# Kernel tuning notes

Measured on AMD Instinct MI355X. Metric: run time of the kernel, lower is better.

## Reference

```python
import jax, jax.numpy as jnp
import numpy as np

ALPHA = 0.2  # LeakyReLU negative slope
NEG_INF = -9e15


def setup_inputs() -> dict:
    key = jax.random.key(0)
    k1, k2, k3, k4 = jax.random.split(key, 4)
    N, IN_F, OUT_F = 8192, 512, 256
    h = jax.random.normal(k1, (N, IN_F), dtype=jnp.float32)
    adj = jax.random.randint(k2, (N, N), 0, 2).astype(jnp.float32)
    # xavier_uniform for torch Linear weights
    limW = float(np.sqrt(6.0 / (IN_F + OUT_F)))
    W = jax.random.uniform(k3, (OUT_F, IN_F), dtype=jnp.float32, minval=-limW, maxval=limW)
    lima = float(np.sqrt(6.0 / (2 * OUT_F + 1)))
    a_vec = jax.random.uniform(k4, (2 * OUT_F,), dtype=jnp.float32, minval=-lima, maxval=lima)
    return {"h": h, "adj": adj, "W": W, "a_vec": a_vec}


def reference(h, adj, W, a_vec):
    # Wh = W(h), torch Linear: h @ W.T  -> [N, out]
    Wh = h @ W.T
    F_out = W.shape[0]
    # e_ij = leakyrelu(a . [Wh_i, Wh_j]) = leakyrelu(a1.Wh_i + a2.Wh_j)
    s_src = Wh @ a_vec[:F_out]   # [N] contribution of row i
    s_dst = Wh @ a_vec[F_out:]   # [N] contribution of col j
    e = jax.nn.leaky_relu(s_src[:, None] + s_dst[None, :], negative_slope=ALPHA)  # [N, N]
    scores = jnp.where(adj > 0, e, jnp.float32(NEG_INF))
    attention = jax.nn.softmax(scores, axis=1)
    # dropout is identity in eval mode
    h_prime = attention @ Wh  # [N, out]
    return h_prime, attention
```

## Files before the change

### kernel.cpp

```cpp
#include <hip/hip_runtime.h>
#include <stdint.h>

#define N_NODES 8192
#define IN_F    512
#define OUT_F   256
#define ALPHA   0.2f

typedef __attribute__((ext_vector_type(8))) short bf16x8;
typedef __attribute__((ext_vector_type(4))) float f32x4;

__device__ __forceinline__ uint32_t f32_to_bf16(float f) {
    union { float f; uint32_t u; } v; v.f = f;
    uint32_t u = v.u;
    return (u + 0x7fffu + ((u >> 16) & 1u)) >> 16;
}

__device__ __forceinline__ void async_copy16(const void* g, void* l) {
    __builtin_amdgcn_global_load_lds(
        (const __attribute__((address_space(1))) uint32_t*)g,
        (__attribute__((address_space(3))) uint32_t*)l, 16, 0, 0);
}

__global__ __launch_bounds__(256) void k0_wvec(
    const float* __restrict__ W, const float* __restrict__ a_vec,
    float* __restrict__ w12)
{
    const int t  = threadIdx.x;
    const int nb = blockIdx.x * 8;
    float a1lo = 0.f, a1hi = 0.f, a2lo = 0.f, a2hi = 0.f;
    #pragma unroll
    for (int q = 0; q < 8; q++) {
        int n = nb + q;
        float lo = W[(size_t)n * IN_F + t];
        float hi = W[(size_t)n * IN_F + t + 256];
        float a1 = a_vec[n], a2 = a_vec[OUT_F + n];
        a1lo = fmaf(lo, a1, a1lo); a1hi = fmaf(hi, a1, a1hi);
        a2lo = fmaf(lo, a2, a2lo); a2hi = fmaf(hi, a2, a2hi);
    }
    atomicAdd(&w12[t], a1lo);       atomicAdd(&w12[t + 256], a1hi);
    atomicAdd(&w12[512 + t], a2lo); atomicAdd(&w12[512 + t + 256], a2hi);
}

__global__ __launch_bounds__(256) void ks_svec(
    const float* __restrict__ h, const float* __restrict__ w12,
    float* __restrict__ s_src, float* __restrict__ s_dst)
{
    __shared__ float sw[1024];
    const int t = threadIdx.x;
    #pragma unroll
    for (int q = 0; q < 4; q++) sw[q * 256 + t] = w12[q * 256 + t];
    __syncthreads();
    const int w = t >> 6, ln = t & 63;
    const int i = blockIdx.x * 4 + w;
    const float* hr = h + (size_t)i * IN_F + ln * 8;
    float4 h0 = *(const float4*)hr;
    float4 h1 = *(const float4*)(hr + 4);
    const float* w1 = sw + ln * 8;
    const float* w2 = sw + 512 + ln * 8;
    float v1 = h0.x*w1[0] + h0.y*w1[1] + h0.z*w1[2] + h0.w*w1[3]
             + h1.x*w1[4] + h1.y*w1[5] + h1.z*w1[6] + h1.w*w1[7];
    float v2 = h0.x*w2[0] + h0.y*w2[1] + h0.z*w2[2] + h0.w*w2[3]
             + h1.x*w2[4] + h1.y*w2[5] + h1.z*w2[6] + h1.w*w2[7];
    #pragma unroll
    for (int off = 32; off >= 1; off >>= 1) {
        v1 += __shfl_xor(v1, off, 64);
        v2 += __shfl_xor(v2, off, 64);
    }
    if (ln == 0) { s_src[i] = v1; s_dst[i] = v2; }
}

__global__ __launch_bounds__(256) void k1_wh_pack(
    const float* __restrict__ h, const float* __restrict__ W,
    uint16_t* __restrict__ whf)
{
    const int n0 = blockIdx.x * 64, i0 = blockIdx.y * 64;
    const int t  = threadIdx.x;
    const int tn = t & 15, tm = t >> 4;

    __shared__ float As[32][68];
    __shared__ float Bs[32][68];

    float acc[4][4];
    #pragma unroll
    for (int i = 0; i < 4; i++)
        #pragma unroll
        for (int j = 0; j < 4; j++) acc[i][j] = 0.f;

    for (int k0 = 0; k0 < IN_F; k0 += 32) {
        __syncthreads();
        #pragma unroll
        for (int q = 0; q < 2; q++) {
            int u   = q * 256 + t;
            int row = u >> 3;
            int kf  = (u & 7) * 4;
            float4 va = *(const float4*)&h[(size_t)(i0 + row) * IN_F + k0 + kf];
            As[kf + 0][row] = va.x; As[kf + 1][row] = va.y;
            As[kf + 2][row] = va.z; As[kf + 3][row] = va.w;
            float4 vb = *(const float4*)&W[(size_t)(n0 + row) * IN_F + k0 + kf];
            Bs[kf + 0][row] = vb.x; Bs[kf + 1][row] = vb.y;
            Bs[kf + 2][row] = vb.z; Bs[kf + 3][row] = vb.w;
        }
        __syncthreads();
        #pragma unroll
        for (int kk = 0; kk < 32; kk++) {
            float a[4], b[4];
            *(float4*)a = *(const float4*)&As[kk][tm * 4];
            *(float4*)b = *(const float4*)&Bs[kk][tn * 4];
            #pragma unroll
            for (int i = 0; i < 4; i++)
                #pragma unroll
                for (int j = 0; j < 4; j++) acc[i][j] = fmaf(a[i], b[j], acc[i][j]);
        }
    }

    #pragma unroll
    for (int ii = 0; ii < 4; ii++) {
        int gr = i0 + tm * 4 + ii;
        int ck = gr >> 5;
        int lr = (gr >> 3) & 3;
        int jj = gr & 7;
        #pragma unroll
        for (int jn = 0; jn < 4; jn++) {
            int gc   = n0 + tn * 4 + jn;
            int c    = ck * 16 + (gc >> 4);
            int lane = (gc & 15) + lr * 16;
            whf[(size_t)c * 512 + lane * 8 + jj] = (uint16_t)f32_to_bf16(acc[ii][jn]);
        }
    }
}

__global__ __launch_bounds__(256) void k2_mask_l(
    const float* __restrict__ adj, const float* __restrict__ s_src,
    const float* __restrict__ s_dst, uint64_t* __restrict__ mask,
    float* __restrict__ l_out)
{
    const int i = blockIdx.x;
    const int t = threadIdx.x, w = t >> 6, ln = t & 63;
    const float si = s_src[i];
    const float4* rowv = (const float4*)(adj + (size_t)i * N_NODES);
    const float4* sdv  = (const float4*)s_dst;
    float acc = 0.f;
    #pragma unroll
    for (int it = 0; it < 8; it++) {
        int jb = it * 4 + w;
        int v4 = jb * 64 + ln;
        float4 a  = rowv[v4];
        float4 sd = sdv[v4];
        uint64_t b0 = __ballot(a.x > 0.f);
        uint64_t b1 = __ballot(a.y > 0.f);
        uint64_t b2 = __ballot(a.z > 0.f);
        uint64_t b3 = __ballot(a.w > 0.f);
        if (ln == 0) {
            uint64_t* mw = mask + (size_t)i * 128 + jb * 4;
            mw[0] = b0; mw[1] = b1; mw[2] = b2; mw[3] = b3;
        }
        float x, e;
        x = si + sd.x; e = fmaxf(x, ALPHA * x); if (a.x > 0.f) acc += __expf(e);
        x = si + sd.y; e = fmaxf(x, ALPHA * x); if (a.y > 0.f) acc += __expf(e);
        x = si + sd.z; e = fmaxf(x, ALPHA * x); if (a.z > 0.f) acc += __expf(e);
        x = si + sd.w; e = fmaxf(x, ALPHA * x); if (a.w > 0.f) acc += __expf(e);
    }
    #pragma unroll
    for (int off = 32; off >= 1; off >>= 1) acc += __shfl_xor(acc, off, 64);
    __shared__ float red[4];
    if (ln == 0) red[w] = acc;
    __syncthreads();
    if (t == 0) l_out[i] = (red[0] + red[1]) + (red[2] + red[3]);
}

__global__ __launch_bounds__(256, 3) void k3_att_gemm(
    const uint64_t* __restrict__ mask, const float* __restrict__ s_src,
    const float* __restrict__ s_dst, const float* __restrict__ l_in,
    const uint16_t* __restrict__ whf, float* __restrict__ att_out,
    float* __restrict__ partial)
{
    const int rb = blockIdx.x, jc = blockIdx.y;
    const int i0 = rb * 32, jbase = jc * 2048;
    const int t = threadIdx.x, w = t >> 6, ln = t & 63;
    const int mh = w & 1, nh = w >> 1;

    __shared__ uint16_t whf_lds[2][8192];
    __shared__ float    sdt[2048];
    __shared__ uint64_t mtab[32 * 33];

    {
        const float4* s4 = (const float4*)(s_dst + jbase);
        ((float4*)sdt)[t * 2]     = s4[t * 2];
        ((float4*)sdt)[t * 2 + 1] = s4[t * 2 + 1];
        int r = t >> 3, c = (t & 7) * 4;
        const uint64_t* mr = mask + (size_t)(i0 + r) * 128 + (jbase >> 8) * 4 + c;
        uint64_t m0 = mr[0], m1 = mr[1], m2 = mr[2], m3 = mr[3];
        uint64_t* md = &mtab[r * 33 + c];
        md[0] = m0; md[1] = m1; md[2] = m2; md[3] = m3;
        const uint16_t* src = whf + ((size_t)(jbase >> 5)) * 8192;
        #pragma unroll
        for (int q = 0; q < 4; q++) {
            int cchunk = w * 4 + q;
            async_copy16(src + (size_t)cchunk * 512 + ln * 8,
                         &whf_lds[0][cchunk * 512]);
        }
        __builtin_amdgcn_sched_barrier(0);
    }

    const int m   = mh * 16 + (ln & 15);
    const int kof = (ln >> 4) * 8;
    const int gi  = i0 + m;

    const float sim = s_src[gi];
    const float il  = 1.0f / l_in[gi];

    f32x4 acc[8];
    #pragma unroll
    for (int b = 0; b < 8; b++) acc[b] = (f32x4){0.f, 0.f, 0.f, 0.f};

    __syncthreads();

    uint64_t mwv[4];

    for (int it = 0; it < 64; it++) {
        const int cur = it & 1;

        if (it < 63) {
            const uint16_t* src =
                whf + ((size_t)(jbase >> 5) + it + 1) * 8192;
            #pragma unroll
            for (int q = 0; q < 4; q++) {
                int cchunk = w * 4 + q;
                async_copy16(src + (size_t)cchunk * 512 + ln * 8,
                             &whf_lds[cur ^ 1][cchunk * 512]);
            }
        }
        __builtin_amdgcn_sched_barrier(0);

        if ((it & 7) == 0) {
            const uint64_t* mp = &mtab[m * 33 + (it >> 3) * 4];
            mwv[0] = mp[0]; mwv[1] = mp[1]; mwv[2] = mp[2]; mwv[3] = mp[3];
        }

        const float* sp = sdt + it * 32 + kof;
        float4 sd0 = *(const float4*)sp;
        float4 sd1 = *(const float4*)(sp + 4);
        float sdv[8] = {sd0.x, sd0.y, sd0.z, sd0.w, sd1.x, sd1.y, sd1.z, sd1.w};

        const int bbase = ((it & 7) << 3) + (kof >> 2);
        float p[8];
        #pragma unroll
        for (int jj = 0; jj < 8; jj++) {
            float x  = sim + sdv[jj];
            float e  = fmaxf(x, ALPHA * x);
            float pe = __expf(e) * il;
            int bidx = bbase + (jj >> 2);
            p[jj] = ((mwv[jj & 3] >> bidx) & 1ull) ? pe : 0.f;
        }

        union { bf16x8 v; uint32_t u[4]; } pk;
        #pragma unroll
        for (int q = 0; q < 4; q++)
            pk.u[q] = f32_to_bf16(p[2 * q]) | (f32_to_bf16(p[2 * q + 1]) << 16);
        bf16x8 af = pk.v;

        const uint16_t* bl = &whf_lds[cur][nh * 8 * 512 + ln * 8];
        #pragma unroll
        for (int nl = 0; nl < 8; nl++) {
            bf16x8 bfr = *(const bf16x8*)(bl + nl * 512);
            acc[nl] = __builtin_amdgcn_mfma_f32_16x16x32_bf16(af, bfr, acc[nl], 0, 0, 0);
        }

        if (nh == 0) {
            float* go = att_out + (size_t)gi * N_NODES + jbase + it * 32 + kof;
            __builtin_nontemporal_store(*(f32x4*)&p[0], (f32x4*)go);
            __builtin_nontemporal_store(*(f32x4*)&p[4], (f32x4*)(go + 4));
        }

        if (nh == 0) asm volatile("s_waitcnt vmcnt(2)" ::: "memory");
        else         asm volatile("s_waitcnt vmcnt(0)" ::: "memory");
        __builtin_amdgcn_s_barrier();
    }

    float* pbase = partial + (size_t)jc * ((size_t)N_NODES * OUT_F);
    const int gr0 = i0 + mh * 16 + (ln >> 4) * 4;
    #pragma unroll
    for (int nl = 0; nl < 8; nl++) {
        int gc = nh * 128 + nl * 16 + (ln & 15);
        #pragma unroll
        for (int r = 0; r < 4; r++)
            pbase[(size_t)(gr0 + r) * OUT_F + gc] = acc[nl][r];
    }
}

__global__ __launch_bounds__(256) void k4_reduce(
    const float* __restrict__ partial, float* __restrict__ hp)
{
    const size_t S = (size_t)N_NODES * OUT_F;
    int idx = (blockIdx.x * 256 + threadIdx.x) * 4;
    float4 a = *(const float4*)(partial + idx);
    float4 b = *(const float4*)(partial + S + idx);
    float4 c = *(const float4*)(partial + 2 * S + idx);
    float4 d = *(const float4*)(partial + 3 * S + idx);
    float4 o;
    o.x = (a.x + b.x) + (c.x + d.x);
    o.y = (a.y + b.y) + (c.y + d.y);
    o.z = (a.z + b.z) + (c.z + d.z);
    o.w = (a.w + b.w) + (c.w + d.w);
    *(float4*)(hp + idx) = o;
}

extern "C" void kernel_launch(void* const* d_in, const int* in_sizes, int n_in,
                              void* d_out, int out_size, void* d_ws, size_t ws_size,
                              hipStream_t stream) {
    (void)in_sizes; (void)n_in; (void)out_size; (void)ws_size;
    const float* h     = (const float*)d_in[0];
    const float* adj   = (const float*)d_in[1];
    const float* W     = (const float*)d_in[2];
    const float* a_vec = (const float*)d_in[3];

    char* ws = (char*)d_ws;
    uint16_t* whf  = (uint16_t*)(ws);
    uint64_t* mask = (uint64_t*)(ws + ((size_t)4 << 20));
    float* partial = (float*)(ws + ((size_t)12 << 20));
    float* w12     = (float*)(ws + ((size_t)44 << 20));
    float* s_src   = (float*)(ws + ((size_t)44 << 20) + 16384);
    float* s_dst   = (float*)(ws + ((size_t)44 << 20) + 16384 + 32768);
    float* l_buf   = (float*)(ws + ((size_t)44 << 20) + 16384 + 65536);

    float* hp  = (float*)d_out;
    float* att = hp + (size_t)N_NODES * OUT_F;

    hipMemsetAsync(w12, 0, 4096, stream);
    k0_wvec<<<32, 256, 0, stream>>>(W, a_vec, w12);
    ks_svec<<<2048, 256, 0, stream>>>(h, w12, s_src, s_dst);
    k1_wh_pack<<<dim3(4, 128), 256, 0, stream>>>(h, W, whf);
    k2_mask_l<<<8192, 256, 0, stream>>>(adj, s_src, s_dst, mask, l_buf);
    k3_att_gemm<<<dim3(256, 4), 256, 0, stream>>>(mask, s_src, s_dst, l_buf, whf, att, partial);
    k4_reduce<<<2048, 256, 0, stream>>>(partial, hp);
}
```

Measured before the change: 727.0 us.

## Move attention matrix writes out of MFMA loop into coalesced epilogue pass

Stops writing the attention probabilities from inside the main MFMA loop, where only half the waves stored scattered 8-float fragments. After the GEMM, all 256 threads recompute the probabilities from LDS-cached s_src, 1/l, s_dst and mask words and write full contiguous rows with float4 nontemporal stores. This is meant to give better-coalesced store traffic and a lighter inner loop. The cost is recomputing every exp a second time, and the stores no longer overlap with MFMA work.

```diff
diff --git a/kernel.cpp b/kernel.cpp
--- a/kernel.cpp
+++ b/kernel.cpp
@@ -182,6 +182,7 @@
     __shared__ uint16_t whf_lds[2][8192];
     __shared__ float    sdt[2048];
     __shared__ uint64_t mtab[32 * 33];
+    __shared__ float    ssrc[32], sinvl[32];
 
     {
         const float4* s4 = (const float4*)(s_dst + jbase);
@@ -192,6 +193,7 @@
         uint64_t m0 = mr[0], m1 = mr[1], m2 = mr[2], m3 = mr[3];
         uint64_t* md = &mtab[r * 33 + c];
         md[0] = m0; md[1] = m1; md[2] = m2; md[3] = m3;
+        if (t < 32) { ssrc[t] = s_src[i0 + t]; sinvl[t] = 1.0f / l_in[i0 + t]; }
         const uint16_t* src = whf + ((size_t)(jbase >> 5)) * 8192;
         #pragma unroll
         for (int q = 0; q < 4; q++) {
@@ -266,25 +268,42 @@
             acc[nl] = __builtin_amdgcn_mfma_f32_16x16x32_bf16(af, bfr, acc[nl], 0, 0, 0);
         }
 
-        if (nh == 0) {
-            float* go = att_out + (size_t)gi * N_NODES + jbase + it * 32 + kof;
-            __builtin_nontemporal_store(*(f32x4*)&p[0], (f32x4*)go);
-            __builtin_nontemporal_store(*(f32x4*)&p[4], (f32x4*)(go + 4));
-        }
-
-        if (nh == 0) asm volatile("s_waitcnt vmcnt(2)" ::: "memory");
-        else         asm volatile("s_waitcnt vmcnt(0)" ::: "memory");
+        asm volatile("s_waitcnt vmcnt(0)" ::: "memory");
         __builtin_amdgcn_s_barrier();
     }
 
-    float* pbase = partial + (size_t)jc * ((size_t)N_NODES * OUT_F);
-    const int gr0 = i0 + mh * 16 + (ln >> 4) * 4;
-    #pragma unroll
-    for (int nl = 0; nl < 8; nl++) {
-        int gc = nh * 128 + nl * 16 + (ln & 15);
-        #pragma unroll
-        for (int r = 0; r < 4; r++)
-            pbase[(size_t)(gr0 + r) * OUT_F + gc] = acc[nl][r];
+    {
+        float* pbase = partial + (size_t)jc * ((size_t)N_NODES * OUT_F);
+        const int gr0 = i0 + mh * 16 + (ln >> 4) * 4;
+        #pragma unroll
+        for (int nl = 0; nl < 8; nl++) {
+            int gc = nh * 128 + nl * 16 + (ln & 15);
+            #pragma unroll
+            for (int r = 0; r < 4; r++)
+                pbase[(size_t)(gr0 + r) * OUT_F + gc] = acc[nl][r];
+        }
+    }
+
+    #pragma unroll 4
+    for (int k = 0; k < 64; k++) {
+        int row = k >> 1;
+        int col = ((k & 1) << 10) + t * 4;
+        float si  = ssrc[row];
+        float ilr = sinvl[row];
+        const uint64_t* mwp = &mtab[row * 33 + ((col >> 8) << 2)];
+        int b = t & 63;
+        float4 sd4 = *(const float4*)&sdt[col];
+        float sdv4[4] = {sd4.x, sd4.y, sd4.z, sd4.w};
+        float o[4];
+        #pragma unroll
+        for (int d = 0; d < 4; d++) {
+            float x  = si + sdv4[d];
+            float e  = fmaxf(x, ALPHA * x);
+            float pe = __expf(e) * ilr;
+            o[d] = ((mwp[d] >> b) & 1ull) ? pe : 0.f;
+        }
+        float* go = att_out + (size_t)(i0 + row) * N_NODES + jbase + col;
+        __builtin_nontemporal_store(*(f32x4*)o, (f32x4*)go);
     }
 }
 
```

After: 626.9 us. 1.16x faster.

## Move attention matrix write into mask kernel and defer normalization in GEMM

Applied to the files above, without the earlier changes.

The dense attention output is now computed and written by the per-row mask/row-sum kernel right after the row sum is known, instead of inside the attention GEMM. The GEMM works on unnormalized exp weights and applies 1/l per row at the epilogue, reads mask bits directly from global memory instead of staging them in LDS, and raises the occupancy hint from 3 to 4. This moves the 256 MB attention store out of the MFMA loop and simplifies its wait logic. In exchange the exp/mask work is done twice, and bf16 rounding now applies to unnormalized values.

```diff
diff --git a/kernel.cpp b/kernel.cpp
--- a/kernel.cpp
+++ b/kernel.cpp
@@ -129,16 +129,20 @@
     }
 }
 
-__global__ __launch_bounds__(256) void k2_mask_l(
+__global__ __launch_bounds__(256) void k2_mask_att(
     const float* __restrict__ adj, const float* __restrict__ s_src,
     const float* __restrict__ s_dst, uint64_t* __restrict__ mask,
-    float* __restrict__ l_out)
+    float* __restrict__ l_out, float* __restrict__ att_out)
 {
     const int i = blockIdx.x;
     const int t = threadIdx.x, w = t >> 6, ln = t & 63;
     const float si = s_src[i];
     const float4* rowv = (const float4*)(adj + (size_t)i * N_NODES);
     const float4* sdv  = (const float4*)s_dst;
+
+    __shared__ uint64_t mtab[128];
+    __shared__ float red[4];
+
     float acc = 0.f;
     #pragma unroll
     for (int it = 0; it < 8; it++) {
@@ -153,6 +157,8 @@
         if (ln == 0) {
             uint64_t* mw = mask + (size_t)i * 128 + jb * 4;
             mw[0] = b0; mw[1] = b1; mw[2] = b2; mw[3] = b3;
+            uint64_t* ml = &mtab[jb * 4];
+            ml[0] = b0; ml[1] = b1; ml[2] = b2; ml[3] = b3;
         }
         float x, e;
         x = si + sd.x; e = fmaxf(x, ALPHA * x); if (a.x > 0.f) acc += __expf(e);
@@ -162,17 +168,39 @@
     }
     #pragma unroll
     for (int off = 32; off >= 1; off >>= 1) acc += __shfl_xor(acc, off, 64);
-    __shared__ float red[4];
     if (ln == 0) red[w] = acc;
     __syncthreads();
-    if (t == 0) l_out[i] = (red[0] + red[1]) + (red[2] + red[3]);
-}
-
-__global__ __launch_bounds__(256, 3) void k3_att_gemm(
+
+    float l = (red[0] + red[1]) + (red[2] + red[3]);
+    if (t == 0) l_out[i] = l;
+    const float il = 1.0f / l;
+
+    float* arow = att_out + (size_t)i * N_NODES;
+    #pragma unroll
+    for (int g = 0; g < 8; g++) {
+        int j0 = g * 1024 + t * 4;
+        int jb = j0 >> 8;
+        const uint64_t* mwp = &mtab[jb * 4];
+        uint64_t m0 = mwp[0], m1 = mwp[1], m2 = mwp[2], m3 = mwp[3];
+        float4 sd4 = sdv[j0 >> 2];
+        float o[4];
+        float x, e;
+        x = si + sd4.x; e = fmaxf(x, ALPHA * x);
+        o[0] = ((m0 >> ln) & 1ull) ? __expf(e) * il : 0.f;
+        x = si + sd4.y; e = fmaxf(x, ALPHA * x);
+        o[1] = ((m1 >> ln) & 1ull) ? __expf(e) * il : 0.f;
+        x = si + sd4.z; e = fmaxf(x, ALPHA * x);
+        o[2] = ((m2 >> ln) & 1ull) ? __expf(e) * il : 0.f;
+        x = si + sd4.w; e = fmaxf(x, ALPHA * x);
+        o[3] = ((m3 >> ln) & 1ull) ? __expf(e) * il : 0.f;
+        *(float4*)(arow + j0) = *(float4*)o;
+    }
+}
+
+__global__ __launch_bounds__(256, 4) void k3_att_gemm(
     const uint64_t* __restrict__ mask, const float* __restrict__ s_src,
     const float* __restrict__ s_dst, const float* __restrict__ l_in,
-    const uint16_t* __restrict__ whf, float* __restrict__ att_out,
-    float* __restrict__ partial)
+    const uint16_t* __restrict__ whf, float* __restrict__ partial)
 {
     const int rb = blockIdx.x, jc = blockIdx.y;
     const int i0 = rb * 32, jbase = jc * 2048;
@@ -181,17 +209,11 @@
 
     __shared__ uint16_t whf_lds[2][8192];
     __shared__ float    sdt[2048];
-    __shared__ uint64_t mtab[32 * 33];
 
     {
         const float4* s4 = (const float4*)(s_dst + jbase);
         ((float4*)sdt)[t * 2]     = s4[t * 2];
         ((float4*)sdt)[t * 2 + 1] = s4[t * 2 + 1];
-        int r = t >> 3, c = (t & 7) * 4;
-        const uint64_t* mr = mask + (size_t)(i0 + r) * 128 + (jbase >> 8) * 4 + c;
-        uint64_t m0 = mr[0], m1 = mr[1], m2 = mr[2], m3 = mr[3];
-        uint64_t* md = &mtab[r * 33 + c];
-        md[0] = m0; md[1] = m1; md[2] = m2; md[3] = m3;
         const uint16_t* src = whf + ((size_t)(jbase >> 5)) * 8192;
         #pragma unroll
         for (int q = 0; q < 4; q++) {
@@ -207,7 +229,6 @@
     const int gi  = i0 + m;
 
     const float sim = s_src[gi];
-    const float il  = 1.0f / l_in[gi];
 
     f32x4 acc[8];
     #pragma unroll
@@ -233,7 +254,8 @@
         __builtin_amdgcn_sched_barrier(0);
 
         if ((it & 7) == 0) {
-            const uint64_t* mp = &mtab[m * 33 + (it >> 3) * 4];
+            const uint64_t* mp =
+                mask + (size_t)gi * 128 + (jbase >> 8) * 4 + (it >> 3) * 4;
             mwv[0] = mp[0]; mwv[1] = mp[1]; mwv[2] = mp[2]; mwv[3] = mp[3];
         }
 
@@ -248,7 +270,7 @@
         for (int jj = 0; jj < 8; jj++) {
             float x  = sim + sdv[jj];
             float e  = fmaxf(x, ALPHA * x);
-            float pe = __expf(e) * il;
+            float pe = __expf(e);
             int bidx = bbase + (jj >> 2);
             p[jj] = ((mwv[jj & 3] >> bidx) & 1ull) ? pe : 0.f;
         }
@@ -266,25 +288,21 @@
             acc[nl] = __builtin_amdgcn_mfma_f32_16x16x32_bf16(af, bfr, acc[nl], 0, 0, 0);
         }
 
-        if (nh == 0) {
-            float* go = att_out + (size_t)gi * N_NODES + jbase + it * 32 + kof;
-            __builtin_nontemporal_store(*(f32x4*)&p[0], (f32x4*)go);
-            __builtin_nontemporal_store(*(f32x4*)&p[4], (f32x4*)(go + 4));
-        }
-
-        if (nh == 0) asm volatile("s_waitcnt vmcnt(2)" ::: "memory");
-        else         asm volatile("s_waitcnt vmcnt(0)" ::: "memory");
+        asm volatile("s_waitcnt vmcnt(0)" ::: "memory");
         __builtin_amdgcn_s_barrier();
     }
 
     float* pbase = partial + (size_t)jc * ((size_t)N_NODES * OUT_F);
     const int gr0 = i0 + mh * 16 + (ln >> 4) * 4;
+    float il4[4];
+    #pragma unroll
+    for (int r = 0; r < 4; r++) il4[r] = 1.0f / l_in[gr0 + r];
     #pragma unroll
     for (int nl = 0; nl < 8; nl++) {
         int gc = nh * 128 + nl * 16 + (ln & 15);
         #pragma unroll
         for (int r = 0; r < 4; r++)
-            pbase[(size_t)(gr0 + r) * OUT_F + gc] = acc[nl][r];
+            pbase[(size_t)(gr0 + r) * OUT_F + gc] = acc[nl][r] * il4[r];
     }
 }
 
@@ -330,7 +348,7 @@
     k0_wvec<<<32, 256, 0, stream>>>(W, a_vec, w12);
     ks_svec<<<2048, 256, 0, stream>>>(h, w12, s_src, s_dst);
     k1_wh_pack<<<dim3(4, 128), 256, 0, stream>>>(h, W, whf);
-    k2_mask_l<<<8192, 256, 0, stream>>>(adj, s_src, s_dst, mask, l_buf);
-    k3_att_gemm<<<dim3(256, 4), 256, 0, stream>>>(mask, s_src, s_dst, l_buf, whf, att, partial);
+    k2_mask_att<<<8192, 256, 0, stream>>>(adj, s_src, s_dst, mask, l_buf, att);
+    k3_att_gemm<<<dim3(256, 4), 256, 0, stream>>>(mask, s_src, s_dst, l_buf, whf, partial);
     k4_reduce<<<2048, 256, 0, stream>>>(partial, hp);
 }
```

New measurement: 612.3 us. 1.19x faster.
